# Optimization experiments

Measured on AMD Instinct MI355X. Metric: run time of the kernel, lower is better.

Reference implementation:

```python
import jax, jax.numpy as jnp
import numpy as np

NEG_INF = -1e30


def setup_inputs() -> dict:
    key = jax.random.key(0)
    kx, km, kq, kk, kv, ko = jax.random.split(key, 6)
    B, D, L = 2, 1024, 2048
    H, DK = 16, 64
    x = jax.random.normal(kx, (B, D, L), dtype=jnp.float32)
    mask = (jax.random.uniform(km, (B, L)) < 0.9).astype(jnp.float32)
    # per-head projection weights, stacked: (H, D, DK); output proj (D, H*DK)==(D, D)
    sq = 1.0 / np.sqrt(D)
    Wq = jax.random.normal(kq, (H, D, DK), dtype=jnp.float32) * sq
    Wk = jax.random.normal(kk, (H, D, DK), dtype=jnp.float32) * sq
    Wv = jax.random.normal(kv, (H, D, DK), dtype=jnp.float32) * sq
    Wo = jax.random.normal(ko, (D, H * DK), dtype=jnp.float32) * sq
    return {"x": x, "mask": mask, "Wq": Wq, "Wk": Wk, "Wv": Wv, "Wo": Wo}


def reference(x, mask, Wq, Wk, Wv, Wo):
    # x: (B, D, L); original transposes to (B, L, D)
    B, D, L = x.shape
    H, _, DK = Wq.shape
    xt = jnp.transpose(x, (0, 2, 1))  # (B, L, D)
    q = jnp.einsum('bld,hdk->bhlk', xt, Wq)
    k = jnp.einsum('bld,hdk->bhlk', xt, Wk)
    v = jnp.einsum('bld,hdk->bhlk', xt, Wv)
    scores = jnp.einsum('bhlk,bhmk->bhlm', q, k) * (1.0 / np.sqrt(DK))
    # masked log-softmax over keys (hmask), squad-style: mask*logit + (1-mask)*-1e30
    hmask = mask[:, None, None, :]  # (B,1,1,Lk)
    masked = hmask * scores + (1.0 - hmask) * NEG_INF
    logp = jax.nn.log_softmax(masked, axis=-1)
    # second softmax over the log-probs, then multiplicative vmask on query dim
    p = jax.nn.softmax(logp, axis=-1) * mask[:, None, :, None]
    heads = jnp.einsum('bhlm,bhmk->bhlk', p, v)  # (B,H,L,DK)
    head = jnp.transpose(heads, (0, 2, 1, 3)).reshape(B, L, H * DK)
    out = jnp.einsum('ble,de->bld', head, Wo)  # matmul(head, Wo) with Wo (D, H*DK)... 
    # NOTE: torch.matmul(head, Wo) treats Wo as (H*DK_in, D_out) only if square; here
    # Wo is (D, H*DK) with D == H*DK, and torch contracts head's last dim with Wo's FIRST dim:
    out = head @ Wo  # (B, L, H*DK) @ (D, H*DK) requires D==H*DK; contracts dim 0 of Wo
    return jnp.transpose(out, (0, 2, 1))  # (B, D, L)


if __name__ == "__main__":
    print(reference(**setup_inputs()).shape)
```

## Files before the change

kernel.cpp:

```cpp
#include <hip/hip_runtime.h>

typedef unsigned short u16;
typedef unsigned long long u64;
typedef short s8v __attribute__((ext_vector_type(8)));
typedef __bf16 bfv8 __attribute__((ext_vector_type(8)));
typedef float f4 __attribute__((ext_vector_type(4)));
typedef u64 u64v2 __attribute__((ext_vector_type(2)));

static constexpr int B = 2, D = 1024, L = 2048, H = 16, DK = 64, E = 1024;
static constexpr float QSCALE = 0.125f * 1.44269504088896340736f;
static constexpr float SMB = -16.0f;

#define DEV __device__ __forceinline__

DEV u16 f2bf(float f) {
  unsigned int u = __float_as_uint(f);
  u += 0x7FFFu + ((u >> 16) & 1u);
  return (u16)(u >> 16);
}
DEV float fexp2(float x) { return __builtin_amdgcn_exp2f(x); }

#define GLD_LDS16(gp, lp)                                                     \
  __builtin_amdgcn_global_load_lds(                                           \
      (const __attribute__((address_space(1))) void*)(gp),                    \
      (__attribute__((address_space(3))) void*)(lp), 16, 0, 0)

__global__ __launch_bounds__(256) void k_prep(
    const float* __restrict__ x, const float* __restrict__ Wq,
    const float* __restrict__ Wk, const float* __restrict__ Wv,
    const float* __restrict__ Wo, u16* __restrict__ xt, u16* __restrict__ Wt,
    u16* __restrict__ WoT) {
  __shared__ u16 t[64][67];
  const int tid = threadIdx.x;
  const int g = blockIdx.x;
  const float* src;
  u16* dst;
  int sld, dld;
  if (g < 1024) {
    const int b = g >> 9, dt = (g >> 5) & 15, lt = g & 31;
    src = x + ((size_t)b * D + dt * 64) * L + lt * 64;
    sld = L;
    dst = xt + ((size_t)b * L + lt * 64) * D + dt * 64;
    dld = D;
  } else if (g < 1792) {
    const int u = g - 1024;
    const int w = u >> 8, h = (u >> 4) & 15, dt = u & 15;
    const float* Ws = (w == 0) ? Wq : ((w == 1) ? Wk : Wv);
    src = Ws + ((size_t)h * D + dt * 64) * DK;
    sld = DK;
    dst = Wt + ((size_t)(w * H + h) * DK) * D + dt * 64;
    dld = D;
  } else {
    const int v = g - 1792;
    const int et = v >> 4, dt = v & 15;
    src = Wo + ((size_t)et * 64) * D + dt * 64;
    sld = D;
    dst = WoT + ((size_t)dt * 64) * E + et * 64;
    dld = E;
  }
  const int r = tid >> 2, c16 = (tid & 3) * 16;
#pragma unroll
  for (int j = 0; j < 16; j += 4) {
    const f4 v4 = *(const f4*)(src + (size_t)r * sld + c16 + j);
    t[r][c16 + j]     = f2bf(v4[0]);
    t[r][c16 + j + 1] = f2bf(v4[1]);
    t[r][c16 + j + 2] = f2bf(v4[2]);
    t[r][c16 + j + 3] = f2bf(v4[3]);
  }
  __syncthreads();
  s8v o0, o1;
#pragma unroll
  for (int i = 0; i < 8; ++i) {
    o0[i] = (short)t[c16 + i][r];
    o1[i] = (short)t[c16 + 8 + i][r];
  }
  *(s8v*)(dst + (size_t)r * dld + c16)     = o0;
  *(s8v*)(dst + (size_t)r * dld + c16 + 8) = o1;
}

template <int AR>
DEV void gemm_tile(const u16* __restrict__ A, const u16* __restrict__ Bt,
                   int arow0, int brow0, u16* As, u16* Bs,
                   f4 (&acc)[AR / 32][4]) {
  const int tid = threadIdx.x;
  const int wid = tid >> 6, lane = tid & 63;
  const int q = lane >> 4, ln = lane & 15;
  const int wr = wid >> 1, wc = wid & 1;
  const int lrow = lane >> 2;
  const int lcg = (lane & 3) ^ ((lane >> 3) & 3);
  const int scA = (q ^ ((ln >> 1) & 3)) * 8;
  constexpr int MT = AR / 32;

  for (int k0 = 0; k0 < 1024; k0 += 32) {
    __syncthreads();
#pragma unroll
    for (int j = 0; j < AR / 64; ++j) {
      const int rb = wid * (AR / 4) + j * 16;
      const u16* gp = A + (size_t)(arow0 + rb + lrow) * 1024 + k0 + lcg * 8;
      GLD_LDS16(gp, As + rb * 32);
    }
#pragma unroll
    for (int j = 0; j < 2; ++j) {
      const int rb = wid * 32 + j * 16;
      const u16* gp = Bt + (size_t)(brow0 + rb + lrow) * 1024 + k0 + lcg * 8;
      GLD_LDS16(gp, Bs + rb * 32);
    }
    __syncthreads();
    bfv8 af[MT], bf[4];
#pragma unroll
    for (int mt = 0; mt < MT; ++mt)
      af[mt] = *(const bfv8*)(As + (wr * (AR / 2) + mt * 16 + ln) * 32 + scA);
#pragma unroll
    for (int nt = 0; nt < 4; ++nt)
      bf[nt] = *(const bfv8*)(Bs + (wc * 64 + nt * 16 + ln) * 32 + scA);
#pragma unroll
    for (int mt = 0; mt < MT; ++mt)
#pragma unroll
      for (int nt = 0; nt < 4; ++nt)
        acc[mt][nt] = __builtin_amdgcn_mfma_f32_16x16x32_bf16(
            af[mt], bf[nt], acc[mt][nt], 0, 0, 0);
  }
}

__global__ __launch_bounds__(256, 2) void k_qkvg(
    const u16* __restrict__ xt, const u16* __restrict__ Wt,
    u16* __restrict__ Q, u16* __restrict__ K, u16* __restrict__ Vt) {
  __shared__ u16 As[128 * 32];
  __shared__ u16 Bs[128 * 32];
  const int bm = blockIdx.x, bn = blockIdx.y;
  f4 acc[4][4];
#pragma unroll
  for (int mt = 0; mt < 4; ++mt)
#pragma unroll
    for (int nt = 0; nt < 4; ++nt) acc[mt][nt] = (f4){0.f, 0.f, 0.f, 0.f};
  gemm_tile<128>(xt, Wt, bm * 128, bn * 128, As, Bs, acc);

  const int tid = threadIdx.x, wid = tid >> 6, lane = tid & 63;
  const int q = lane >> 4, ln = lane & 15;
  const int wr = wid >> 1, wc = wid & 1;
  const int h2 = bn * 2 + wc;
  const int wsel = h2 >> 4, h = h2 & 15;
  const int b = bm >> 4;
  const int lbase = (bm & 15) * 128 + wr * 64;
  if (wsel == 0) {
    u16* dst = Q + (size_t)(b * H + h) * L * DK;
#pragma unroll
    for (int mt = 0; mt < 4; ++mt)
#pragma unroll
      for (int nt = 0; nt < 4; ++nt)
#pragma unroll
        for (int r = 0; r < 4; ++r)
          dst[(size_t)(lbase + mt * 16 + q * 4 + r) * DK + nt * 16 + ln] =
              f2bf(acc[mt][nt][r] * QSCALE);
  } else if (wsel == 1) {
    u16* dst = K + (size_t)(b * H + h) * L * DK;
#pragma unroll
    for (int mt = 0; mt < 4; ++mt)
#pragma unroll
      for (int nt = 0; nt < 4; ++nt)
#pragma unroll
        for (int r = 0; r < 4; ++r)
          dst[(size_t)(lbase + mt * 16 + q * 4 + r) * DK + nt * 16 + ln] =
              f2bf(acc[mt][nt][r]);
  } else {
    u16* dst = Vt + (size_t)(b * H + h) * DK * L;
#pragma unroll
    for (int mt = 0; mt < 4; ++mt)
#pragma unroll
      for (int nt = 0; nt < 4; ++nt)
#pragma unroll
        for (int r = 0; r < 4; ++r) {
          const int l = lbase + mt * 16 + q * 4 + r;
          dst[(size_t)(nt * 16 + ln) * L + (l & ~63) + ((l & 15) << 2) +
              ((l >> 4) & 3)] = f2bf(acc[mt][nt][r]);
        }
  }
}

__global__ __launch_bounds__(256, 4) void k_attn(
    const u16* __restrict__ Q, const u16* __restrict__ K,
    const u16* __restrict__ Vt, const float* __restrict__ mask,
    u16* __restrict__ Hd) {
  __shared__ u16 kt[64 * 72];
  __shared__ u16 vt[64 * 72];
  __shared__ float mf[L];
  __shared__ u16 p_lds[4][16 * 72];
  const int lt = blockIdx.x, h = blockIdx.y, b = blockIdx.z;
  const int tid = threadIdx.x;
  const int w = tid >> 6, lane = tid & 63, q = lane >> 4, ln = lane & 15;
  for (int i = tid; i < L; i += 256) mf[i] = mask[(size_t)b * L + i];

  const int bh = b * H + h;
  const u16* Qp = Q + (size_t)bh * L * DK;
  const u16* Kp = K + (size_t)bh * L * DK;
  const u16* Vp = Vt + (size_t)bh * DK * L;
  const int lq = lt * 64 + w * 16;

  const bfv8 qf0 = *(const bfv8*)(Qp + (size_t)(lq + ln) * DK + q * 8);
  const bfv8 qf1 = *(const bfv8*)(Qp + (size_t)(lq + ln) * DK + 32 + q * 8);

  f4 o[4];
  float l_r[4];
#pragma unroll
  for (int i = 0; i < 4; ++i) {
    o[i] = (f4){0.f, 0.f, 0.f, 0.f};
    l_r[i] = 0.f;
  }
  u16* pw = &p_lds[w][0];
  const int srow = tid >> 3;
  const int sc = (tid & 7) * 8;

  for (int m0 = 0; m0 < L; m0 += 64) {
    __syncthreads();
    {
      const s8v k0v = *(const s8v*)(Kp + (size_t)(m0 + srow) * DK + sc);
      const s8v k1v = *(const s8v*)(Kp + (size_t)(m0 + srow + 32) * DK + sc);
      const s8v v0v = *(const s8v*)(Vp + (size_t)srow * L + m0 + sc);
      const s8v v1v = *(const s8v*)(Vp + (size_t)(srow + 32) * L + m0 + sc);
      *(s8v*)&kt[srow * 72 + sc] = k0v;
      *(s8v*)&kt[(srow + 32) * 72 + sc] = k1v;
      *(s8v*)&vt[srow * 72 + sc] = v0v;
      *(s8v*)&vt[(srow + 32) * 72 + sc] = v1v;
    }
    __syncthreads();

    bfv8 kf0[4], kf1[4];
    float kmf[4];
#pragma unroll
    for (int nt = 0; nt < 4; ++nt) {
      const int row = nt * 16 + ln;
      kf0[nt] = *(const bfv8*)(kt + row * 72 + q * 8);
      kf1[nt] = *(const bfv8*)(kt + row * 72 + 32 + q * 8);
      kmf[nt] = mf[m0 + row];
    }
    f4 s[4];
#pragma unroll
    for (int nt = 0; nt < 4; ++nt) {
      f4 a = (f4){SMB, SMB, SMB, SMB};
      a = __builtin_amdgcn_mfma_f32_16x16x32_bf16(qf0, kf0[nt], a, 0, 0, 0);
      a = __builtin_amdgcn_mfma_f32_16x16x32_bf16(qf1, kf1[nt], a, 0, 0, 0);
      s[nt] = a;
    }
#pragma unroll
    for (int r = 0; r < 4; ++r) {
      const float p0 = fexp2(s[0][r]) * kmf[0];
      const float p1 = fexp2(s[1][r]) * kmf[1];
      const float p2 = fexp2(s[2][r]) * kmf[2];
      const float p3 = fexp2(s[3][r]) * kmf[3];
      l_r[r] += (p0 + p1) + (p2 + p3);
      const u64 pk = (u64)f2bf(p0) | ((u64)f2bf(p1) << 16) |
                     ((u64)f2bf(p2) << 32) | ((u64)f2bf(p3) << 48);
      *(u64*)(pw + (q * 4 + r) * 72 + ln * 4) = pk;
    }
    u64v2 r0, r1;
    r0[0] = *(const u64*)(pw + ln * 72 + q * 8);
    r0[1] = *(const u64*)(pw + ln * 72 + q * 8 + 4);
    r1[0] = *(const u64*)(pw + ln * 72 + 32 + q * 8);
    r1[1] = *(const u64*)(pw + ln * 72 + 32 + q * 8 + 4);
    const bfv8 pa0 = __builtin_bit_cast(bfv8, r0);
    const bfv8 pa1 = __builtin_bit_cast(bfv8, r1);
#pragma unroll
    for (int nt = 0; nt < 4; ++nt) {
      const int row = nt * 16 + ln;
      const bfv8 vf0 = *(const bfv8*)(vt + row * 72 + q * 8);
      const bfv8 vf1 = *(const bfv8*)(vt + row * 72 + 32 + q * 8);
      o[nt] = __builtin_amdgcn_mfma_f32_16x16x32_bf16(pa0, vf0, o[nt], 0, 0, 0);
      o[nt] = __builtin_amdgcn_mfma_f32_16x16x32_bf16(pa1, vf1, o[nt], 0, 0, 0);
    }
  }
#pragma unroll
  for (int r = 0; r < 4; ++r) {
#pragma unroll
    for (int off = 1; off < 16; off <<= 1)
      l_r[r] += __shfl_xor(l_r[r], off, 16);
    const float qm = mf[lq + q * 4 + r];
    l_r[r] = (qm != 0.0f) ? (1.0f / l_r[r]) : 0.0f;
  }
#pragma unroll
  for (int nt = 0; nt < 4; ++nt)
#pragma unroll
    for (int r = 0; r < 4; ++r)
      Hd[(size_t)(b * L + lq + q * 4 + r) * E + h * DK + nt * 16 + ln] =
          f2bf(o[nt][r] * l_r[r]);
}

__global__ __launch_bounds__(256, 2) void k_projg(const u16* __restrict__ WoT,
                                                  const u16* __restrict__ Hd,
                                                  float* __restrict__ out) {
  __shared__ u16 As[64 * 32];
  __shared__ u16 Bs[128 * 32];
  const int bm = blockIdx.x, bn = blockIdx.y;
  f4 acc[2][4];
#pragma unroll
  for (int mt = 0; mt < 2; ++mt)
#pragma unroll
    for (int nt = 0; nt < 4; ++nt) acc[mt][nt] = (f4){0.f, 0.f, 0.f, 0.f};
  gemm_tile<64>(WoT, Hd, bm * 64, bn * 128, As, Bs, acc);

  const int tid = threadIdx.x, wid = tid >> 6, lane = tid & 63;
  const int q = lane >> 4, ln = lane & 15;
  const int wr = wid >> 1, wc = wid & 1;
#pragma unroll
  for (int mt = 0; mt < 2; ++mt)
#pragma unroll
    for (int nt = 0; nt < 4; ++nt)
#pragma unroll
      for (int r = 0; r < 4; ++r) {
        const int d = bm * 64 + wr * 32 + mt * 16 + q * 4 + r;
        const int n = bn * 128 + wc * 64 + nt * 16 + ln;
        const int bb = n >> 11, l = n & 2047;
        out[((size_t)(bb * D + d)) * L + l] = acc[mt][nt][r];
      }
}

extern "C" void kernel_launch(void* const* d_in, const int* in_sizes, int n_in,
                              void* d_out, int out_size, void* d_ws,
                              size_t ws_size, hipStream_t stream) {
  const float* x    = (const float*)d_in[0];
  const float* mask = (const float*)d_in[1];
  const float* Wq   = (const float*)d_in[2];
  const float* Wk   = (const float*)d_in[3];
  const float* Wv   = (const float*)d_in[4];
  const float* Wo   = (const float*)d_in[5];
  u16* ws = (u16*)d_ws;
  u16* Qws  = ws;
  u16* Kws  = ws + 4194304;
  u16* Vtws = ws + 8388608;
  u16* WoTw = ws + 12582912;
  u16* Wtws = ws + 13631488;
  u16* xtws = ws + 16777216;
  u16* Hdws = ws + 16777216;

  k_prep<<<2048, 256, 0, stream>>>(x, Wq, Wk, Wv, Wo, xtws, Wtws, WoTw);
  k_qkvg<<<dim3(32, 24), 256, 0, stream>>>(xtws, Wtws, Qws, Kws, Vtws);
  k_attn<<<dim3(32, 16, 2), 256, 0, stream>>>(Qws, Kws, Vtws, mask, Hdws);
  k_projg<<<dim3(16, 32), 256, 0, stream>>>(WoTw, Hdws, (float*)d_out);
}
```

Before: 201.4 us.

## Double attention query tile per wave, use direct global-to-LDS loads with XOR swizzle

The attention kernel now gives each wave 32 query rows instead of 16, so every K/V fragment read from LDS feeds two MFMA tiles and each K/V tile is loaded half as many times overall. K/V staging switches from register round-trips to global_load_lds with an XOR-swizzled unpadded layout to avoid bank conflicts. bf16 packing uses the paired conversion intrinsic, and the launch bounds change (attn 4->2 waves hint, qkvg 2->3). The cost is more registers per thread and half as many attention blocks (512), which lowers occupancy and latency hiding.

```diff
diff --git a/kernel.cpp b/kernel.cpp
--- a/kernel.cpp
+++ b/kernel.cpp
@@ -1,6 +1,8 @@
 #include <hip/hip_runtime.h>
+#include <hip/hip_bf16.h>
 
 typedef unsigned short u16;
+typedef unsigned int u32;
 typedef unsigned long long u64;
 typedef short s8v __attribute__((ext_vector_type(8)));
 typedef __bf16 bfv8 __attribute__((ext_vector_type(8)));
@@ -19,6 +21,12 @@
   return (u16)(u >> 16);
 }
 DEV float fexp2(float x) { return __builtin_amdgcn_exp2f(x); }
+DEV u32 pkbf(float a, float b) {
+  __hip_bfloat162 h = __float22bfloat162_rn(float2{a, b});
+  u32 r;
+  __builtin_memcpy(&r, &h, 4);
+  return r;
+}
 
 #define GLD_LDS16(gp, lp)                                                     \
   __builtin_amdgcn_global_load_lds(                                           \
@@ -122,7 +130,7 @@
   }
 }
 
-__global__ __launch_bounds__(256, 2) void k_qkvg(
+__global__ __launch_bounds__(256, 3) void k_qkvg(
     const u16* __restrict__ xt, const u16* __restrict__ Wt,
     u16* __restrict__ Q, u16* __restrict__ K, u16* __restrict__ Vt) {
   __shared__ u16 As[128 * 32];
@@ -177,14 +185,14 @@
   }
 }
 
-__global__ __launch_bounds__(256, 4) void k_attn(
+__global__ __launch_bounds__(256, 2) void k_attn(
     const u16* __restrict__ Q, const u16* __restrict__ K,
     const u16* __restrict__ Vt, const float* __restrict__ mask,
     u16* __restrict__ Hd) {
-  __shared__ u16 kt[64 * 72];
-  __shared__ u16 vt[64 * 72];
+  __shared__ u16 kt[64 * 64];
+  __shared__ u16 vt[64 * 64];
   __shared__ float mf[L];
-  __shared__ u16 p_lds[4][16 * 72];
+  __shared__ u16 p_lds[4][32 * 72];
   const int lt = blockIdx.x, h = blockIdx.y, b = blockIdx.z;
   const int tid = threadIdx.x;
   const int w = tid >> 6, lane = tid & 63, q = lane >> 4, ln = lane & 15;
@@ -194,94 +202,112 @@
   const u16* Qp = Q + (size_t)bh * L * DK;
   const u16* Kp = K + (size_t)bh * L * DK;
   const u16* Vp = Vt + (size_t)bh * DK * L;
-  const int lq = lt * 64 + w * 16;
-
-  const bfv8 qf0 = *(const bfv8*)(Qp + (size_t)(lq + ln) * DK + q * 8);
-  const bfv8 qf1 = *(const bfv8*)(Qp + (size_t)(lq + ln) * DK + 32 + q * 8);
-
-  f4 o[4];
-  float l_r[4];
-#pragma unroll
-  for (int i = 0; i < 4; ++i) {
-    o[i] = (f4){0.f, 0.f, 0.f, 0.f};
-    l_r[i] = 0.f;
-  }
+  const int lq = lt * 128 + w * 32;
+
+  bfv8 qf[2][2];
+#pragma unroll
+  for (int mt = 0; mt < 2; ++mt) {
+    qf[mt][0] = *(const bfv8*)(Qp + (size_t)(lq + mt * 16 + ln) * DK + q * 8);
+    qf[mt][1] =
+        *(const bfv8*)(Qp + (size_t)(lq + mt * 16 + ln) * DK + 32 + q * 8);
+  }
+
+  f4 o[2][4];
+  float l_r[2][4];
+#pragma unroll
+  for (int mt = 0; mt < 2; ++mt)
+#pragma unroll
+    for (int i = 0; i < 4; ++i) {
+      o[mt][i] = (f4){0.f, 0.f, 0.f, 0.f};
+      l_r[mt][i] = 0.f;
+    }
   u16* pw = &p_lds[w][0];
-  const int srow = tid >> 3;
-  const int sc = (tid & 7) * 8;
+
+  const int lrow = lane >> 3;
+  const int lc = (lane & 7) ^ lrow;
+  const int fr0 = w * 16 + lrow, fr1 = w * 16 + 8 + lrow;
+  const int c0 = (q ^ (ln & 7)) * 8;
+  const int c1 = ((q + 4) ^ (ln & 7)) * 8;
 
   for (int m0 = 0; m0 < L; m0 += 64) {
     __syncthreads();
-    {
-      const s8v k0v = *(const s8v*)(Kp + (size_t)(m0 + srow) * DK + sc);
-      const s8v k1v = *(const s8v*)(Kp + (size_t)(m0 + srow + 32) * DK + sc);
-      const s8v v0v = *(const s8v*)(Vp + (size_t)srow * L + m0 + sc);
-      const s8v v1v = *(const s8v*)(Vp + (size_t)(srow + 32) * L + m0 + sc);
-      *(s8v*)&kt[srow * 72 + sc] = k0v;
-      *(s8v*)&kt[(srow + 32) * 72 + sc] = k1v;
-      *(s8v*)&vt[srow * 72 + sc] = v0v;
-      *(s8v*)&vt[(srow + 32) * 72 + sc] = v1v;
-    }
+    GLD_LDS16(Kp + (size_t)(m0 + fr0) * DK + lc * 8, kt + (w * 16) * 64);
+    GLD_LDS16(Kp + (size_t)(m0 + fr1) * DK + lc * 8, kt + (w * 16 + 8) * 64);
+    GLD_LDS16(Vp + (size_t)fr0 * L + m0 + lc * 8, vt + (w * 16) * 64);
+    GLD_LDS16(Vp + (size_t)fr1 * L + m0 + lc * 8, vt + (w * 16 + 8) * 64);
     __syncthreads();
 
-    bfv8 kf0[4], kf1[4];
-    float kmf[4];
+    float km[4];
+    f4 s[2][4];
 #pragma unroll
     for (int nt = 0; nt < 4; ++nt) {
       const int row = nt * 16 + ln;
-      kf0[nt] = *(const bfv8*)(kt + row * 72 + q * 8);
-      kf1[nt] = *(const bfv8*)(kt + row * 72 + 32 + q * 8);
-      kmf[nt] = mf[m0 + row];
-    }
-    f4 s[4];
-#pragma unroll
-    for (int nt = 0; nt < 4; ++nt) {
-      f4 a = (f4){SMB, SMB, SMB, SMB};
-      a = __builtin_amdgcn_mfma_f32_16x16x32_bf16(qf0, kf0[nt], a, 0, 0, 0);
-      a = __builtin_amdgcn_mfma_f32_16x16x32_bf16(qf1, kf1[nt], a, 0, 0, 0);
-      s[nt] = a;
-    }
-#pragma unroll
-    for (int r = 0; r < 4; ++r) {
-      const float p0 = fexp2(s[0][r]) * kmf[0];
-      const float p1 = fexp2(s[1][r]) * kmf[1];
-      const float p2 = fexp2(s[2][r]) * kmf[2];
-      const float p3 = fexp2(s[3][r]) * kmf[3];
-      l_r[r] += (p0 + p1) + (p2 + p3);
-      const u64 pk = (u64)f2bf(p0) | ((u64)f2bf(p1) << 16) |
-                     ((u64)f2bf(p2) << 32) | ((u64)f2bf(p3) << 48);
-      *(u64*)(pw + (q * 4 + r) * 72 + ln * 4) = pk;
-    }
-    u64v2 r0, r1;
-    r0[0] = *(const u64*)(pw + ln * 72 + q * 8);
-    r0[1] = *(const u64*)(pw + ln * 72 + q * 8 + 4);
-    r1[0] = *(const u64*)(pw + ln * 72 + 32 + q * 8);
-    r1[1] = *(const u64*)(pw + ln * 72 + 32 + q * 8 + 4);
-    const bfv8 pa0 = __builtin_bit_cast(bfv8, r0);
-    const bfv8 pa1 = __builtin_bit_cast(bfv8, r1);
+      const bfv8 kf0 = *(const bfv8*)(kt + row * 64 + c0);
+      const bfv8 kf1 = *(const bfv8*)(kt + row * 64 + c1);
+      km[nt] = mf[m0 + row];
+#pragma unroll
+      for (int mt = 0; mt < 2; ++mt) {
+        f4 a = (f4){SMB, SMB, SMB, SMB};
+        a = __builtin_amdgcn_mfma_f32_16x16x32_bf16(qf[mt][0], kf0, a, 0, 0, 0);
+        a = __builtin_amdgcn_mfma_f32_16x16x32_bf16(qf[mt][1], kf1, a, 0, 0, 0);
+        s[mt][nt] = a;
+      }
+    }
+#pragma unroll
+    for (int mt = 0; mt < 2; ++mt)
+#pragma unroll
+      for (int r = 0; r < 4; ++r) {
+        const float p0 = fexp2(s[mt][0][r]) * km[0];
+        const float p1 = fexp2(s[mt][1][r]) * km[1];
+        const float p2 = fexp2(s[mt][2][r]) * km[2];
+        const float p3 = fexp2(s[mt][3][r]) * km[3];
+        l_r[mt][r] += (p0 + p1) + (p2 + p3);
+        const u64 pk = (u64)pkbf(p0, p1) | ((u64)pkbf(p2, p3) << 32);
+        *(u64*)(pw + (mt * 16 + q * 4 + r) * 72 + ln * 4) = pk;
+      }
+    bfv8 pa[2][2];
+#pragma unroll
+    for (int mt = 0; mt < 2; ++mt) {
+      u64v2 r0, r1;
+      r0[0] = *(const u64*)(pw + (mt * 16 + ln) * 72 + q * 8);
+      r0[1] = *(const u64*)(pw + (mt * 16 + ln) * 72 + q * 8 + 4);
+      r1[0] = *(const u64*)(pw + (mt * 16 + ln) * 72 + 32 + q * 8);
+      r1[1] = *(const u64*)(pw + (mt * 16 + ln) * 72 + 32 + q * 8 + 4);
+      pa[mt][0] = __builtin_bit_cast(bfv8, r0);
+      pa[mt][1] = __builtin_bit_cast(bfv8, r1);
+    }
 #pragma unroll
     for (int nt = 0; nt < 4; ++nt) {
       const int row = nt * 16 + ln;
-      const bfv8 vf0 = *(const bfv8*)(vt + row * 72 + q * 8);
-      const bfv8 vf1 = *(const bfv8*)(vt + row * 72 + 32 + q * 8);
-      o[nt] = __builtin_amdgcn_mfma_f32_16x16x32_bf16(pa0, vf0, o[nt], 0, 0, 0);
-      o[nt] = __builtin_amdgcn_mfma_f32_16x16x32_bf16(pa1, vf1, o[nt], 0, 0, 0);
-    }
-  }
-#pragma unroll
-  for (int r = 0; r < 4; ++r) {
-#pragma unroll
-    for (int off = 1; off < 16; off <<= 1)
-      l_r[r] += __shfl_xor(l_r[r], off, 16);
-    const float qm = mf[lq + q * 4 + r];
-    l_r[r] = (qm != 0.0f) ? (1.0f / l_r[r]) : 0.0f;
-  }
-#pragma unroll
-  for (int nt = 0; nt < 4; ++nt)
-#pragma unroll
-    for (int r = 0; r < 4; ++r)
-      Hd[(size_t)(b * L + lq + q * 4 + r) * E + h * DK + nt * 16 + ln] =
-          f2bf(o[nt][r] * l_r[r]);
+      const bfv8 vf0 = *(const bfv8*)(vt + row * 64 + c0);
+      const bfv8 vf1 = *(const bfv8*)(vt + row * 64 + c1);
+#pragma unroll
+      for (int mt = 0; mt < 2; ++mt) {
+        o[mt][nt] = __builtin_amdgcn_mfma_f32_16x16x32_bf16(pa[mt][0], vf0,
+                                                            o[mt][nt], 0, 0, 0);
+        o[mt][nt] = __builtin_amdgcn_mfma_f32_16x16x32_bf16(pa[mt][1], vf1,
+                                                            o[mt][nt], 0, 0, 0);
+      }
+    }
+  }
+#pragma unroll
+  for (int mt = 0; mt < 2; ++mt)
+#pragma unroll
+    for (int r = 0; r < 4; ++r) {
+#pragma unroll
+      for (int off = 1; off < 16; off <<= 1)
+        l_r[mt][r] += __shfl_xor(l_r[mt][r], off, 16);
+      const float qm = mf[lq + mt * 16 + q * 4 + r];
+      l_r[mt][r] = (qm != 0.0f) ? (1.0f / l_r[mt][r]) : 0.0f;
+    }
+#pragma unroll
+  for (int mt = 0; mt < 2; ++mt)
+#pragma unroll
+    for (int nt = 0; nt < 4; ++nt)
+#pragma unroll
+      for (int r = 0; r < 4; ++r)
+        Hd[(size_t)(b * L + lq + mt * 16 + q * 4 + r) * E + h * DK + nt * 16 +
+           ln] = f2bf(o[mt][nt][r] * l_r[mt][r]);
 }
 
 __global__ __launch_bounds__(256, 2) void k_projg(const u16* __restrict__ WoT,
@@ -333,6 +359,6 @@
 
   k_prep<<<2048, 256, 0, stream>>>(x, Wq, Wk, Wv, Wo, xtws, Wtws, WoTw);
   k_qkvg<<<dim3(32, 24), 256, 0, stream>>>(xtws, Wtws, Qws, Kws, Vtws);
-  k_attn<<<dim3(32, 16, 2), 256, 0, stream>>>(Qws, Kws, Vtws, mask, Hdws);
+  k_attn<<<dim3(16, 16, 2), 256, 0, stream>>>(Qws, Kws, Vtws, mask, Hdws);
   k_projg<<<dim3(16, 32), 256, 0, stream>>>(WoTw, Hdws, (float*)d_out);
 }
```

After: 191.0 us. -5.2%, faster.

## Restructure attention loop: transposed S, register-resident P, double-buffered async K/V loads

Applied to the files above, without the earlier changes.

The attention kernel now computes S transposed (K as the A operand), so the exp'd probabilities feed the PV MFMA straight from registers via 16x16x16 bf16 instructions. This removes the LDS round-trip for P. K/V tiles are double-buffered using global_load_lds with XOR swizzling, dropping one barrier per iteration. The key mask is folded into the MFMA accumulator init as an additive bias rather than a multiply. The V store in the QKV kernel is simplified to packed 64-bit writes, its launch bound is raised to 3 waves, and the grid order is changed so heads vary fastest. The additive mask bias relies on exp2 underflowing to exactly zero, and the double buffering uses more LDS.

```diff
diff --git a/kernel.cpp b/kernel.cpp
--- a/kernel.cpp
+++ b/kernel.cpp
@@ -1,15 +1,18 @@
 #include <hip/hip_runtime.h>
+#include <hip/hip_bf16.h>
 
 typedef unsigned short u16;
+typedef unsigned int u32;
 typedef unsigned long long u64;
 typedef short s8v __attribute__((ext_vector_type(8)));
+typedef short s4v __attribute__((ext_vector_type(4)));
 typedef __bf16 bfv8 __attribute__((ext_vector_type(8)));
 typedef float f4 __attribute__((ext_vector_type(4)));
-typedef u64 u64v2 __attribute__((ext_vector_type(2)));
 
 static constexpr int B = 2, D = 1024, L = 2048, H = 16, DK = 64, E = 1024;
 static constexpr float QSCALE = 0.125f * 1.44269504088896340736f;
 static constexpr float SMB = -16.0f;
+static constexpr float MASKB = -12000.0f;
 
 #define DEV __device__ __forceinline__
 
@@ -19,6 +22,16 @@
   return (u16)(u >> 16);
 }
 DEV float fexp2(float x) { return __builtin_amdgcn_exp2f(x); }
+DEV u32 pkbf(float a, float b) {
+  __hip_bfloat162 h = __float22bfloat162_rn(float2{a, b});
+  u32 r;
+  __builtin_memcpy(&r, &h, 4);
+  return r;
+}
+
+DEV f4 mfma16(s4v a, s4v b, f4 c) {
+  return __builtin_amdgcn_mfma_f32_16x16x16bf16_1k(a, b, c, 0, 0, 0);
+}
 
 #define GLD_LDS16(gp, lp)                                                     \
   __builtin_amdgcn_global_load_lds(                                           \
@@ -96,14 +109,14 @@
 #pragma unroll
     for (int j = 0; j < AR / 64; ++j) {
       const int rb = wid * (AR / 4) + j * 16;
-      const u16* gp = A + (size_t)(arow0 + rb + lrow) * 1024 + k0 + lcg * 8;
-      GLD_LDS16(gp, As + rb * 32);
+      GLD_LDS16(A + (size_t)(arow0 + rb + lrow) * 1024 + k0 + lcg * 8,
+                As + rb * 32);
     }
 #pragma unroll
     for (int j = 0; j < 2; ++j) {
       const int rb = wid * 32 + j * 16;
-      const u16* gp = Bt + (size_t)(brow0 + rb + lrow) * 1024 + k0 + lcg * 8;
-      GLD_LDS16(gp, Bs + rb * 32);
+      GLD_LDS16(Bt + (size_t)(brow0 + rb + lrow) * 1024 + k0 + lcg * 8,
+                Bs + rb * 32);
     }
     __syncthreads();
     bfv8 af[MT], bf[4];
@@ -122,7 +135,7 @@
   }
 }
 
-__global__ __launch_bounds__(256, 2) void k_qkvg(
+__global__ __launch_bounds__(256, 3) void k_qkvg(
     const u16* __restrict__ xt, const u16* __restrict__ Wt,
     u16* __restrict__ Q, u16* __restrict__ K, u16* __restrict__ Vt) {
   __shared__ u16 As[128 * 32];
@@ -167,13 +180,12 @@
 #pragma unroll
     for (int mt = 0; mt < 4; ++mt)
 #pragma unroll
-      for (int nt = 0; nt < 4; ++nt)
-#pragma unroll
-        for (int r = 0; r < 4; ++r) {
-          const int l = lbase + mt * 16 + q * 4 + r;
-          dst[(size_t)(nt * 16 + ln) * L + (l & ~63) + ((l & 15) << 2) +
-              ((l >> 4) & 3)] = f2bf(acc[mt][nt][r]);
-        }
+      for (int nt = 0; nt < 4; ++nt) {
+        const u64 pk = (u64)pkbf(acc[mt][nt][0], acc[mt][nt][1]) |
+                       ((u64)pkbf(acc[mt][nt][2], acc[mt][nt][3]) << 32);
+        *(u64*)(dst + (size_t)(nt * 16 + ln) * L + lbase + mt * 16 + q * 4) =
+            pk;
+      }
   }
 }
 
@@ -181,14 +193,14 @@
     const u16* __restrict__ Q, const u16* __restrict__ K,
     const u16* __restrict__ Vt, const float* __restrict__ mask,
     u16* __restrict__ Hd) {
-  __shared__ u16 kt[64 * 72];
-  __shared__ u16 vt[64 * 72];
-  __shared__ float mf[L];
-  __shared__ u16 p_lds[4][16 * 72];
-  const int lt = blockIdx.x, h = blockIdx.y, b = blockIdx.z;
+  __shared__ u16 kt[2][64 * 64];
+  __shared__ u16 vt[2][64 * 64];
+  __shared__ __align__(16) float mb[L];
+  const int h = blockIdx.x, lt = blockIdx.y, b = blockIdx.z;
   const int tid = threadIdx.x;
   const int w = tid >> 6, lane = tid & 63, q = lane >> 4, ln = lane & 15;
-  for (int i = tid; i < L; i += 256) mf[i] = mask[(size_t)b * L + i];
+  for (int i = tid; i < L; i += 256)
+    mb[i] = (mask[(size_t)b * L + i] != 0.0f) ? SMB : MASKB;
 
   const int bh = b * H + h;
   const u16* Qp = Q + (size_t)bh * L * DK;
@@ -199,89 +211,80 @@
   const bfv8 qf0 = *(const bfv8*)(Qp + (size_t)(lq + ln) * DK + q * 8);
   const bfv8 qf1 = *(const bfv8*)(Qp + (size_t)(lq + ln) * DK + 32 + q * 8);
 
-  f4 o[4];
-  float l_r[4];
-#pragma unroll
-  for (int i = 0; i < 4; ++i) {
-    o[i] = (f4){0.f, 0.f, 0.f, 0.f};
-    l_r[i] = 0.f;
-  }
-  u16* pw = &p_lds[w][0];
-  const int srow = tid >> 3;
-  const int sc = (tid & 7) * 8;
-
-  for (int m0 = 0; m0 < L; m0 += 64) {
+  const int lrow = lane >> 3;
+  const int lc = (lane & 7) ^ lrow;
+  const int fr0 = w * 16 + lrow, fr1 = fr0 + 8;
+  const int c0 = (q ^ (ln & 7)) * 8;
+  const int c1 = ((q + 4) ^ (ln & 7)) * 8;
+
+  auto stage = [&](int m0, int bufi) {
+    GLD_LDS16(Kp + (size_t)(m0 + fr0) * DK + lc * 8, &kt[bufi][(w * 16) * 64]);
+    GLD_LDS16(Kp + (size_t)(m0 + fr1) * DK + lc * 8,
+              &kt[bufi][(w * 16 + 8) * 64]);
+    GLD_LDS16(Vp + (size_t)fr0 * L + m0 + lc * 8, &vt[bufi][(w * 16) * 64]);
+    GLD_LDS16(Vp + (size_t)fr1 * L + m0 + lc * 8, &vt[bufi][(w * 16 + 8) * 64]);
+  };
+
+  f4 ot[4];
+#pragma unroll
+  for (int i = 0; i < 4; ++i) ot[i] = (f4){0.f, 0.f, 0.f, 0.f};
+  float lp = 0.f;
+
+  stage(0, 0);
+  for (int it = 0; it < L / 64; ++it) {
+    const int m0 = it * 64;
     __syncthreads();
-    {
-      const s8v k0v = *(const s8v*)(Kp + (size_t)(m0 + srow) * DK + sc);
-      const s8v k1v = *(const s8v*)(Kp + (size_t)(m0 + srow + 32) * DK + sc);
-      const s8v v0v = *(const s8v*)(Vp + (size_t)srow * L + m0 + sc);
-      const s8v v1v = *(const s8v*)(Vp + (size_t)(srow + 32) * L + m0 + sc);
-      *(s8v*)&kt[srow * 72 + sc] = k0v;
-      *(s8v*)&kt[(srow + 32) * 72 + sc] = k1v;
-      *(s8v*)&vt[srow * 72 + sc] = v0v;
-      *(s8v*)&vt[(srow + 32) * 72 + sc] = v1v;
-    }
-    __syncthreads();
-
-    bfv8 kf0[4], kf1[4];
-    float kmf[4];
+    if (it + 1 < L / 64) stage(m0 + 64, (it + 1) & 1);
+    const u16* ktc = &kt[it & 1][0];
+    const u16* vtc = &vt[it & 1][0];
+
+    f4 s[4];
 #pragma unroll
     for (int nt = 0; nt < 4; ++nt) {
-      const int row = nt * 16 + ln;
-      kf0[nt] = *(const bfv8*)(kt + row * 72 + q * 8);
-      kf1[nt] = *(const bfv8*)(kt + row * 72 + 32 + q * 8);
-      kmf[nt] = mf[m0 + row];
-    }
-    f4 s[4];
+      const int krow = nt * 16 + ln;
+      const bfv8 kf0 = *(const bfv8*)(ktc + krow * 64 + c0);
+      const bfv8 kf1 = *(const bfv8*)(ktc + krow * 64 + c1);
+      f4 a = *(const f4*)(mb + m0 + nt * 16 + q * 4);
+      a = __builtin_amdgcn_mfma_f32_16x16x32_bf16(kf0, qf0, a, 0, 0, 0);
+      a = __builtin_amdgcn_mfma_f32_16x16x32_bf16(kf1, qf1, a, 0, 0, 0);
+      s[nt] = a;
+    }
+    s4v pb[4];
 #pragma unroll
     for (int nt = 0; nt < 4; ++nt) {
-      f4 a = (f4){SMB, SMB, SMB, SMB};
-      a = __builtin_amdgcn_mfma_f32_16x16x32_bf16(qf0, kf0[nt], a, 0, 0, 0);
-      a = __builtin_amdgcn_mfma_f32_16x16x32_bf16(qf1, kf1[nt], a, 0, 0, 0);
-      s[nt] = a;
-    }
-#pragma unroll
-    for (int r = 0; r < 4; ++r) {
-      const float p0 = fexp2(s[0][r]) * kmf[0];
-      const float p1 = fexp2(s[1][r]) * kmf[1];
-      const float p2 = fexp2(s[2][r]) * kmf[2];
-      const float p3 = fexp2(s[3][r]) * kmf[3];
-      l_r[r] += (p0 + p1) + (p2 + p3);
-      const u64 pk = (u64)f2bf(p0) | ((u64)f2bf(p1) << 16) |
-                     ((u64)f2bf(p2) << 32) | ((u64)f2bf(p3) << 48);
-      *(u64*)(pw + (q * 4 + r) * 72 + ln * 4) = pk;
-    }
-    u64v2 r0, r1;
-    r0[0] = *(const u64*)(pw + ln * 72 + q * 8);
-    r0[1] = *(const u64*)(pw + ln * 72 + q * 8 + 4);
-    r1[0] = *(const u64*)(pw + ln * 72 + 32 + q * 8);
-    r1[1] = *(const u64*)(pw + ln * 72 + 32 + q * 8 + 4);
-    const bfv8 pa0 = __builtin_bit_cast(bfv8, r0);
-    const bfv8 pa1 = __builtin_bit_cast(bfv8, r1);
-#pragma unroll
-    for (int nt = 0; nt < 4; ++nt) {
-      const int row = nt * 16 + ln;
-      const bfv8 vf0 = *(const bfv8*)(vt + row * 72 + q * 8);
-      const bfv8 vf1 = *(const bfv8*)(vt + row * 72 + 32 + q * 8);
-      o[nt] = __builtin_amdgcn_mfma_f32_16x16x32_bf16(pa0, vf0, o[nt], 0, 0, 0);
-      o[nt] = __builtin_amdgcn_mfma_f32_16x16x32_bf16(pa1, vf1, o[nt], 0, 0, 0);
-    }
-  }
-#pragma unroll
-  for (int r = 0; r < 4; ++r) {
-#pragma unroll
-    for (int off = 1; off < 16; off <<= 1)
-      l_r[r] += __shfl_xor(l_r[r], off, 16);
-    const float qm = mf[lq + q * 4 + r];
-    l_r[r] = (qm != 0.0f) ? (1.0f / l_r[r]) : 0.0f;
-  }
-#pragma unroll
-  for (int nt = 0; nt < 4; ++nt)
-#pragma unroll
-    for (int r = 0; r < 4; ++r)
-      Hd[(size_t)(b * L + lq + q * 4 + r) * E + h * DK + nt * 16 + ln] =
-          f2bf(o[nt][r] * l_r[r]);
+      const float p0 = fexp2(s[nt][0]);
+      const float p1 = fexp2(s[nt][1]);
+      const float p2 = fexp2(s[nt][2]);
+      const float p3 = fexp2(s[nt][3]);
+      lp += (p0 + p1) + (p2 + p3);
+      const u64 pk = (u64)pkbf(p0, p1) | ((u64)pkbf(p2, p3) << 32);
+      pb[nt] = __builtin_bit_cast(s4v, pk);
+    }
+#pragma unroll
+    for (int dt = 0; dt < 4; ++dt) {
+      const int vrow = dt * 16 + ln;
+      const int vbase = vrow * 64 + (q & 1) * 4;
+      const int rx = vrow & 7;
+      f4 a = ot[dt];
+#pragma unroll
+      for (int kc = 0; kc < 4; ++kc) {
+        const s4v av =
+            *(const s4v*)(vtc + vbase + (((kc * 2 + (q >> 1)) ^ rx) * 8));
+        a = mfma16(av, pb[kc], a);
+      }
+      ot[dt] = a;
+    }
+  }
+  lp += __shfl_xor(lp, 16);
+  lp += __shfl_xor(lp, 32);
+  const float linv = (mb[lq + ln] > -100.0f) ? (1.0f / lp) : 0.0f;
+#pragma unroll
+  for (int dt = 0; dt < 4; ++dt) {
+    const u64 pk =
+        (u64)pkbf(ot[dt][0] * linv, ot[dt][1] * linv) |
+        ((u64)pkbf(ot[dt][2] * linv, ot[dt][3] * linv) << 32);
+    *(u64*)(Hd + (size_t)(b * L + lq + ln) * E + h * DK + dt * 16 + q * 4) = pk;
+  }
 }
 
 __global__ __launch_bounds__(256, 2) void k_projg(const u16* __restrict__ WoT,
@@ -333,6 +336,6 @@
 
   k_prep<<<2048, 256, 0, stream>>>(x, Wq, Wk, Wv, Wo, xtws, Wtws, WoTw);
   k_qkvg<<<dim3(32, 24), 256, 0, stream>>>(xtws, Wtws, Qws, Kws, Vtws);
-  k_attn<<<dim3(32, 16, 2), 256, 0, stream>>>(Qws, Kws, Vtws, mask, Hdws);
+  k_attn<<<dim3(16, 32, 2), 256, 0, stream>>>(Qws, Kws, Vtws, mask, Hdws);
   k_projg<<<dim3(16, 32), 256, 0, stream>>>(WoTw, Hdws, (float*)d_out);
 }
```

Result: faster. 189.6 us (-5.9%).
